# Kernel tuning notes

Measured on AMD Instinct MI355X. Metric: run time of the kernel, lower is better.

Reference implementation:

```python
import jax, jax.numpy as jnp
import numpy as np
from jax.ops import segment_sum

N_NODES = 50000
N_EDGES = 800000
N_GRAPHS = 256
F_IN, F_HID, N_HID, N_OUT = 64, 128, 512, 256


def setup_inputs() -> dict:
    key = jax.random.key(0)
    ks = jax.random.split(key, 12)
    x = jax.random.normal(ks[0], (N_NODES, F_IN), dtype=jnp.float32)
    edge_index = jax.random.randint(ks[1], (2, N_EDGES), 0, N_NODES, dtype=jnp.int64)
    batch = jnp.sort(jax.random.randint(ks[2], (N_NODES,), 0, N_GRAPHS, dtype=jnp.int64))
    def lin(k, fan_in, fan_out):
        s = 1.0 / np.sqrt(fan_in)
        return jax.random.uniform(k, (fan_in, fan_out), jnp.float32, -s, s)
    return {
        "x": x, "edge_index": edge_index, "batch": batch,
        "W0": lin(ks[3], F_IN, F_HID), "b0": jnp.zeros((F_HID,), jnp.float32),
        "W1": lin(ks[4], F_HID, F_HID), "b1": jnp.zeros((F_HID,), jnp.float32),
        "W2": lin(ks[5], F_HID, F_HID), "b2": jnp.zeros((F_HID,), jnp.float32),
        "Wm1": lin(ks[6], F_HID, N_HID), "bm1": jnp.zeros((N_HID,), jnp.float32),
        "Wm2": lin(ks[7], N_HID, N_OUT), "bm2": jnp.zeros((N_OUT,), jnp.float32),
    }


def _gcn_norm(edge_index, num_nodes):
    # PyG GCNConv default: add self-loops, symmetric D^{-1/2} A D^{-1/2} norm.
    loop = jnp.arange(num_nodes, dtype=edge_index.dtype)
    src = jnp.concatenate([edge_index[0], loop])
    dst = jnp.concatenate([edge_index[1], loop])
    deg = segment_sum(jnp.ones_like(src, dtype=jnp.float32), dst, num_segments=num_nodes)
    dis = jnp.where(deg > 0, jax.lax.rsqrt(jnp.maximum(deg, 1.0)), 0.0)
    norm = dis[src] * dis[dst]
    return src, dst, norm


def _gcn_conv(x, W, b, src, dst, norm, num_nodes):
    h = x @ W                                  # [N, F_out]
    msg = norm[:, None] * h[src]               # edge-wise gather  [E+N, F_out]
    out = segment_sum(msg, dst, num_segments=num_nodes)  # scatter-add
    return out + b


def reference(x, edge_index, batch, W0, b0, W1, b1, W2, b2, Wm1, bm1, Wm2, bm2):
    n = x.shape[0]
    src, dst, norm = _gcn_norm(edge_index, n)
    h = jax.nn.relu(_gcn_conv(x, W0, b0, src, dst, norm, n))
    h = jax.nn.relu(_gcn_conv(h, W1, b1, src, dst, norm, n))
    h = _gcn_conv(h, W2, b2, src, dst, norm, n)
    # global_mean_pool over graphs
    counts = segment_sum(jnp.ones((n,), jnp.float32), batch, num_segments=N_GRAPHS)
    g = segment_sum(h, batch, num_segments=N_GRAPHS) / jnp.maximum(counts, 1.0)[:, None]
    # mol_mlp: Linear -> ReLU -> Linear
    g = jax.nn.relu(g @ Wm1 + bm1)
    return g @ Wm2 + bm2
```

## Files before the change

### kernel.cpp

```cpp
#include <hip/hip_runtime.h>
#include <hip/hip_bf16.h>
#include <math.h>
#include <stdint.h>

#define N_NODES 50000
#define N_PAD   50048
#define N_EDGES 800000
#define N_GRAPHS 256
#define F_IN 64
#define F_HID 128
#define N_HID 512
#define N_OUT 256
#define CSR_CAP (N_EDGES + 16 * N_NODES)

#define NBKT   196
#define BKT_S  6144
#define EPB    3328
#define NBIN_BLK ((N_EDGES + EPB - 1) / EPB)
#define DUMMY_NODE N_NODES

using bf16x8 = __attribute__((ext_vector_type(8))) short;
using f32x4  = __attribute__((ext_vector_type(4))) float;

__device__ __forceinline__ unsigned int bf16pair(float a, float b) {
    unsigned int ua = __float_as_uint(a);
    unsigned int ub = __float_as_uint(b);
    ua += 0x7fffu + ((ua >> 16) & 1u);
    ub += 0x7fffu + ((ub >> 16) & 1u);
    return (ua >> 16) | (ub & 0xffff0000u);
}
__device__ __forceinline__ float bf16lo(unsigned int u) { return __uint_as_float(u << 16); }
__device__ __forceinline__ float bf16hi(unsigned int u) { return __uint_as_float(u & 0xffff0000u); }

__device__ __forceinline__ void acc8(float* a, uint4 r) {
    a[0] += bf16lo(r.x);  a[1] += bf16hi(r.x);
    a[2] += bf16lo(r.y);  a[3] += bf16hi(r.y);
    a[4] += bf16lo(r.z);  a[5] += bf16hi(r.z);
    a[6] += bf16lo(r.w);  a[7] += bf16hi(r.w);
}

__global__ void cvt_all(const float* __restrict__ in, const float* __restrict__ dis,
                        unsigned int* __restrict__ xb,
                        const float* __restrict__ W0, unsigned short* __restrict__ W0Tb,
                        const float* __restrict__ W1, unsigned short* __restrict__ W1Tb) {
    const int NX = N_NODES * F_IN / 4;
    int idx = blockIdx.x * blockDim.x + threadIdx.x;
    if (idx < NX) {
        int node = idx >> 4;
        float d = dis[node];
        float4 v = ((const float4*)in)[idx];
        ((uint2*)xb)[idx] = make_uint2(bf16pair(d * v.x, d * v.y),
                                       bf16pair(d * v.z, d * v.w));
        if (idx < 16)
            ((uint2*)xb)[(size_t)N_NODES * 16 + idx] = make_uint2(0u, 0u);
    } else {
        int j = idx - NX;
        const int N0 = F_IN * 128;
        const int N1 = F_HID * 128;
        if (j < N0) {
            int k = j >> 7, n = j & 127;
            unsigned int u = __float_as_uint(W0[j]);
            u += 0x7fffu + ((u >> 16) & 1u);
            W0Tb[n * F_IN + k] = (unsigned short)(u >> 16);
        } else if (j < N0 + N1) {
            int jj = j - N0;
            int k = jj >> 7, n = jj & 127;
            unsigned int u = __float_as_uint(W1[jj]);
            u += 0x7fffu + ((u >> 16) & 1u);
            W1Tb[n * F_HID + k] = (unsigned short)(u >> 16);
        }
    }
}

__global__ __launch_bounds__(256) void bin_edges(const int* __restrict__ ei,
                                                 int* __restrict__ bucketCur,
                                                 unsigned int* __restrict__ binned) {
    __shared__ int hist[NBKT];
    __shared__ int lbase[NBKT];
    __shared__ int lcur[NBKT];
    __shared__ int gbase[NBKT];
    __shared__ int scn[256];
    __shared__ unsigned int staging[EPB];
    int tid = threadIdx.x;
    int base = blockIdx.x * EPB;
    int cnt = N_EDGES - base; if (cnt > EPB) cnt = EPB;
    if (tid < NBKT) hist[tid] = 0;
    __syncthreads();
    unsigned int pk[13]; int nk = 0;
#pragma unroll
    for (int u = 0; u < 13; ++u) {
        int e = base + u * 256 + tid;
        if (u * 256 + tid < cnt) {
            unsigned int s = (unsigned int)ei[e];
            unsigned int d = (unsigned int)ei[N_EDGES + e];
            unsigned int b = d >> 8;
            pk[nk++] = (b << 24) | (s << 8) | (d & 255u);
        }
    }
    for (int u = 0; u < nk; ++u) atomicAdd(&hist[pk[u] >> 24], 1);
    __syncthreads();
    int h = (tid < NBKT) ? hist[tid] : 0;
    scn[tid] = h;
    __syncthreads();
    for (int off = 1; off < 256; off <<= 1) {
        int t = (tid >= off) ? scn[tid - off] : 0;
        __syncthreads();
        scn[tid] += t;
        __syncthreads();
    }
    if (tid < NBKT) { int e0 = scn[tid] - h; lbase[tid] = e0; lcur[tid] = e0; }
    __syncthreads();
    for (int u = 0; u < nk; ++u) {
        int pos = atomicAdd(&lcur[pk[u] >> 24], 1);
        staging[pos] = pk[u];
    }
    if (tid < NBKT && hist[tid] > 0)
        gbase[tid] = atomicAdd(&bucketCur[tid], hist[tid]);
    __syncthreads();
    for (int k = tid; k < cnt; k += 256) {
        unsigned int v = staging[k];
        int b = v >> 24;
        binned[(size_t)b * BKT_S + gbase[b] + (k - lbase[b])] = v & 0xffffffu;
    }
}

__global__ __launch_bounds__(256) void bucket_deg(const unsigned int* __restrict__ binned,
                                                  const int* __restrict__ bucketCur,
                                                  int* __restrict__ degs,
                                                  float* __restrict__ dis,
                                                  int* __restrict__ localOff,
                                                  int* __restrict__ bucketAligned) {
    __shared__ int hist[256];
    __shared__ int tsum[256];
    int b = blockIdx.x;
    int tid = threadIdx.x;
    int node0 = b << 8;
    hist[tid] = 0;
    __syncthreads();
    int cnt = bucketCur[b];
    const unsigned int* bb = &binned[(size_t)b * BKT_S];
    for (int k = tid; k < cnt; k += 256)
        atomicAdd(&hist[bb[k] & 255u], 1);
    __syncthreads();
    int d = hist[tid];
    int s = (d + 15) & ~15;
    tsum[tid] = s;
    __syncthreads();
    for (int off = 1; off < 256; off <<= 1) {
        int t = (tid >= off) ? tsum[tid - off] : 0;
        __syncthreads();
        tsum[tid] += t;
        __syncthreads();
    }
    int excl = tsum[tid] - s;
    int node = node0 + tid;
    if (node < N_NODES) {
        degs[node] = d;
        dis[node] = rsqrtf((float)(d + 1));
        localOff[node] = excl;
    }
    if (tid == 255) bucketAligned[b] = tsum[255];
}

__global__ __launch_bounds__(256) void scatter_local(const unsigned int* __restrict__ binned,
                                                     const int* __restrict__ bucketCur,
                                                     const int* __restrict__ bucketAligned,
                                                     const int* __restrict__ localOff,
                                                     int* __restrict__ offsets,
                                                     unsigned short* __restrict__ csr) {
    __shared__ int lcur[256];
    __shared__ int sc[256];
    __shared__ int s_csrB, s_tot;
    int b = blockIdx.x;
    int tid = threadIdx.x;
    sc[tid] = (tid < NBKT) ? bucketAligned[tid] : 0;
    __syncthreads();
    for (int off = 1; off < 256; off <<= 1) {
        int t = (tid >= off) ? sc[tid - off] : 0;
        __syncthreads();
        sc[tid] += t;
        __syncthreads();
    }
    if (tid == 0) {
        int incl = sc[b];
        int mine = bucketAligned[b];
        s_csrB = incl - mine;
        s_tot  = mine;
    }
    __syncthreads();
    int csrB = s_csrB;
    int tot  = s_tot;
    int node = (b << 8) + tid;
    int lo = (node < N_NODES) ? localOff[node] : 0;
    lcur[tid] = lo;
    if (node < N_NODES) offsets[node] = csrB + lo;
    uint4 dv = make_uint4(0xC350C350u, 0xC350C350u, 0xC350C350u, 0xC350C350u);
    uint4* cp = (uint4*)(csr + csrB);
    for (int k = tid; k < (tot >> 3); k += 256) cp[k] = dv;
    __syncthreads();
    int cnt = bucketCur[b];
    const unsigned int* bb = &binned[(size_t)b * BKT_S];
    for (int k = tid; k < cnt; k += 256) {
        unsigned int v = bb[k];
        int dl = v & 255u;
        int p = atomicAdd(&lcur[dl], 1);
        csr[csrB + p] = (unsigned short)(v >> 8);
    }
}

template <int K, bool BIASRELU, bool DISSCALE>
__global__ __launch_bounds__(256) void gemm_mfma(const unsigned short* __restrict__ Ab,
                                                 const unsigned short* __restrict__ WTb,
                                                 const float* __restrict__ bias,
                                                 const float* __restrict__ disv,
                                                 unsigned int* __restrict__ outb, int M) {
    int wv = threadIdx.x >> 6;
    int lane = threadIdx.x & 63;
    int m = lane & 15;
    int quad = lane >> 4;
    int row0 = blockIdx.x * 64 + wv * 16;
    f32x4 acc[8];
#pragma unroll
    for (int t = 0; t < 8; ++t) acc[t] = (f32x4){0.f, 0.f, 0.f, 0.f};
#pragma unroll
    for (int ks = 0; ks < K; ks += 32) {
        bf16x8 af = *(const bf16x8*)&Ab[(size_t)(row0 + m) * K + ks + quad * 8];
#pragma unroll
        for (int t = 0; t < 8; ++t) {
            bf16x8 bf = *(const bf16x8*)&WTb[(size_t)(t * 16 + m) * K + ks + quad * 8];
            acc[t] = __builtin_amdgcn_mfma_f32_16x16x32_bf16(af, bf, acc[t], 0, 0, 0);
        }
    }
    float dr[4];
#pragma unroll
    for (int r = 0; r < 4; ++r) {
        int row = row0 + quad * 4 + r;
        dr[r] = DISSCALE ? ((row < M) ? disv[row] : 0.f) : 1.f;
    }
#pragma unroll
    for (int t = 0; t < 8; ++t) {
        int col = t * 16 + m;
        float bcol = 0.f;
        if (BIASRELU) bcol = bias[col];
#pragma unroll
        for (int r = 0; r < 4; ++r) {
            float v = acc[t][r];
            if (BIASRELU) v = fmaxf(v + bcol, 0.f);
            if (DISSCALE) v = v * dr[r];
            float vn = __shfl_xor(v, 1, 64);
            if ((m & 1) == 0) {
                int row = row0 + quad * 4 + r;
                if (row < M)
                    outb[(size_t)row * 64 + (col >> 1)] = bf16pair(v, vn);
                else
                    outb[(size_t)row * 64 + (col >> 1)] = 0u;
            }
        }
    }
}

template <bool RELU, bool BIAS, bool SCALEOUT>
__global__ __launch_bounds__(256) void aggregate128b(const uint4* __restrict__ hb4,
                                                     const int* __restrict__ offsets,
                                                     const int* __restrict__ degs,
                                                     const unsigned short* __restrict__ csr,
                                                     const float* __restrict__ dis,
                                                     const float* __restrict__ bias,
                                                     unsigned int* __restrict__ outb) {
    int wave = threadIdx.x >> 6;
    int lane = threadIdx.x & 63;
    int i = blockIdx.x * 4 + wave;
    int sub = lane >> 4;
    int q   = lane & 15;
    if (i >= N_NODES) {
        if (i == N_NODES && sub == 0)
            ((uint4*)outb)[(size_t)N_NODES * 16 + q] = make_uint4(0u, 0u, 0u, 0u);
        return;
    }
    float a[8];
#pragma unroll
    for (int k = 0; k < 8; ++k) a[k] = 0.f;
    int j = offsets[i];
    int e1 = j + ((degs[i] + 15) & ~15);
    for (; j < e1; j += 16) {
        uint2 w = *(const uint2*)&csr[j + 4 * sub];
        int s0 = w.x & 0xffff, s1 = w.x >> 16;
        int s2 = w.y & 0xffff, s3 = w.y >> 16;
        uint4 r0 = hb4[(size_t)s0 * 16 + q];
        uint4 r1 = hb4[(size_t)s1 * 16 + q];
        uint4 r2 = hb4[(size_t)s2 * 16 + q];
        uint4 r3 = hb4[(size_t)s3 * 16 + q];
        acc8(a, r0); acc8(a, r1); acc8(a, r2); acc8(a, r3);
    }
#pragma unroll
    for (int k = 0; k < 8; ++k) a[k] += __shfl_xor(a[k], 16, 64);
#pragma unroll
    for (int k = 0; k < 8; ++k) a[k] += __shfl_xor(a[k], 32, 64);
    uint4 su = hb4[(size_t)i * 16 + q];
    acc8(a, su);
    float dii = dis[i];
#pragma unroll
    for (int k = 0; k < 8; ++k) a[k] *= dii;
    if (BIAS) {
        float4 b0 = ((const float4*)bias)[2 * q];
        float4 b1 = ((const float4*)bias)[2 * q + 1];
        a[0] += b0.x; a[1] += b0.y; a[2] += b0.z; a[3] += b0.w;
        a[4] += b1.x; a[5] += b1.y; a[6] += b1.z; a[7] += b1.w;
    }
    if (RELU) {
#pragma unroll
        for (int k = 0; k < 8; ++k) a[k] = fmaxf(a[k], 0.f);
    }
    if (sub == 0) {
        float sc = SCALEOUT ? dii : 1.f;
        ((uint4*)outb)[(size_t)i * 16 + q] =
            make_uint4(bf16pair(sc * a[0], sc * a[1]), bf16pair(sc * a[2], sc * a[3]),
                       bf16pair(sc * a[4], sc * a[5]), bf16pair(sc * a[6], sc * a[7]));
    }
}

__global__ __launch_bounds__(256) void aggregate_xb(const uint4* __restrict__ xb4,
                                                    const float* __restrict__ x,
                                                    const int* __restrict__ offsets,
                                                    const int* __restrict__ degs,
                                                    const unsigned short* __restrict__ csr,
                                                    const float* __restrict__ dis,
                                                    unsigned int* __restrict__ outb) {
    int wave = threadIdx.x >> 6;
    int lane = threadIdx.x & 63;
    int i = blockIdx.x * 4 + wave;
    int sub = lane >> 3;
    int q   = lane & 7;
    if (i >= N_NODES) {
        if (i == N_NODES && sub == 0)
            ((uint4*)outb)[(size_t)N_NODES * 8 + q] = make_uint4(0u, 0u, 0u, 0u);
        return;
    }
    float a[8];
#pragma unroll
    for (int k = 0; k < 8; ++k) a[k] = 0.f;
    int j = offsets[i];
    int e1 = j + ((degs[i] + 15) & ~15);
    for (; j < e1; j += 16) {
        unsigned int w = *(const unsigned int*)&csr[j + 2 * sub];
        int s0 = w & 0xffff, s1 = w >> 16;
        uint4 r0 = xb4[(size_t)s0 * 8 + q];
        uint4 r1 = xb4[(size_t)s1 * 8 + q];
        acc8(a, r0); acc8(a, r1);
    }
#pragma unroll
    for (int k = 0; k < 8; ++k) a[k] += __shfl_xor(a[k], 8, 64);
#pragma unroll
    for (int k = 0; k < 8; ++k) a[k] += __shfl_xor(a[k], 16, 64);
#pragma unroll
    for (int k = 0; k < 8; ++k) a[k] += __shfl_xor(a[k], 32, 64);
    float dii = dis[i];
    float d2 = dii * dii;
    float4 sx0 = ((const float4*)x)[(size_t)i * 16 + 2 * q];
    float4 sx1 = ((const float4*)x)[(size_t)i * 16 + 2 * q + 1];
    a[0] = dii * a[0] + d2 * sx0.x;  a[1] = dii * a[1] + d2 * sx0.y;
    a[2] = dii * a[2] + d2 * sx0.z;  a[3] = dii * a[3] + d2 * sx0.w;
    a[4] = dii * a[4] + d2 * sx1.x;  a[5] = dii * a[5] + d2 * sx1.y;
    a[6] = dii * a[6] + d2 * sx1.z;  a[7] = dii * a[7] + d2 * sx1.w;
    if (sub == 0)
        ((uint4*)outb)[(size_t)i * 8 + q] =
            make_uint4(bf16pair(a[0], a[1]), bf16pair(a[2], a[3]),
                       bf16pair(a[4], a[5]), bf16pair(a[6], a[7]));
}

__global__ __launch_bounds__(128) void pool16(const unsigned int* __restrict__ hb,
                                              const int* __restrict__ batch,
                                              float* __restrict__ g_acc,
                                              float* __restrict__ g_cnt) {
    const int NB = 16;
    int base = blockIdx.x * NB;
    int f = threadIdx.x;
    int uidx = f >> 1;
    bool hi = f & 1;
    float acc = 0.f;
    int cur = -1, cnt = 0;
    for (int n = 0; n < NB; ++n) {
        int i = base + n;
        if (i >= N_NODES) break;
        int b = batch[i];
        if (b != cur) {
            if (cur >= 0) {
                atomicAdd(&g_acc[(size_t)cur * F_HID + f], acc);
                if (f == 0) atomicAdd(&g_cnt[cur], (float)cnt);
            }
            cur = b; acc = 0.f; cnt = 0;
        }
        unsigned int u = hb[(size_t)i * 64 + uidx];
        acc += hi ? bf16hi(u) : bf16lo(u);
        cnt++;
    }
    if (cur >= 0) {
        atomicAdd(&g_acc[(size_t)cur * F_HID + f], acc);
        if (f == 0) atomicAdd(&g_cnt[cur], (float)cnt);
    }
}

__global__ __launch_bounds__(512) void fused_mlp(const float* __restrict__ g_acc,
                                                 const float* __restrict__ g_cnt,
                                                 const float* __restrict__ W2,
                                                 const float* __restrict__ b2,
                                                 const float* __restrict__ Wm1,
                                                 const float* __restrict__ bm1,
                                                 const float* __restrict__ Wm2,
                                                 const float* __restrict__ bm2,
                                                 float* __restrict__ out) {
    __shared__ float pool_row[F_HID];
    __shared__ float g2row[F_HID];
    __shared__ float hid[N_HID];
    int g = blockIdx.x;
    int t = threadIdx.x;
    if (t < F_HID) {
        float c = g_cnt[g];
        pool_row[t] = g_acc[(size_t)g * F_HID + t] / fmaxf(c, 1.0f);
    }
    __syncthreads();
    if (t < F_HID) {
        float acc = b2[t];
        for (int k = 0; k < F_HID; ++k) acc += pool_row[k] * W2[(size_t)k * F_HID + t];
        g2row[t] = acc;
    }
    __syncthreads();
    {
        float acc = bm1[t];
        for (int k = 0; k < F_HID; ++k) acc += g2row[k] * Wm1[(size_t)k * N_HID + t];
        hid[t] = fmaxf(acc, 0.f);
    }
    __syncthreads();
    if (t < N_OUT) {
        float acc = bm2[t];
        for (int k = 0; k < N_HID; ++k) acc += hid[k] * Wm2[(size_t)k * N_OUT + t];
        out[(size_t)g * N_OUT + t] = acc;
    }
}

extern "C" void kernel_launch(void* const* d_in, const int* in_sizes, int n_in,
                              void* d_out, int out_size, void* d_ws, size_t ws_size,
                              hipStream_t stream) {
    const float* x   = (const float*)d_in[0];
    const int* ei    = (const int*)d_in[1];
    const int* batch = (const int*)d_in[2];
    const float* W0 = (const float*)d_in[3];  const float* b0 = (const float*)d_in[4];
    const float* W1 = (const float*)d_in[5];  const float* b1 = (const float*)d_in[6];
    const float* W2 = (const float*)d_in[7];  const float* b2 = (const float*)d_in[8];
    const float* Wm1 = (const float*)d_in[9];  const float* bm1 = (const float*)d_in[10];
    const float* Wm2 = (const float*)d_in[11]; const float* bm2 = (const float*)d_in[12];

    char* p = (char*)d_ws;
    auto alloc = [&](size_t bytes) -> char* {
        char* r = p;
        p += (bytes + 255) & ~(size_t)255;
        return r;
    };
    int*   bucketCur = (int*)alloc(NBKT * 4);
    float* g_acc  = (float*)alloc((size_t)N_GRAPHS * F_HID * 4);
    float* g_cnt  = (float*)alloc(N_GRAPHS * 4);
    size_t zero_bytes = (size_t)(p - (char*)bucketCur);
    unsigned int* binned = (unsigned int*)alloc((size_t)NBKT * BKT_S * 4);
    int*   bucketAligned = (int*)alloc(NBKT * 4);
    int*   offsets = (int*)alloc((size_t)N_NODES * 4);
    int*   degs    = (int*)alloc((size_t)N_NODES * 4);
    int*   localOff = (int*)alloc((size_t)N_NODES * 4);
    float* dis     = (float*)alloc((size_t)N_NODES * 4);
    unsigned short* csr = (unsigned short*)alloc((size_t)CSR_CAP * 2 + 32);
    unsigned int* xb     = (unsigned int*)alloc((size_t)N_PAD * F_IN / 2 * 4);
    unsigned int* axb    = (unsigned int*)alloc((size_t)N_PAD * F_IN / 2 * 4);
    unsigned int* h_ab   = (unsigned int*)alloc((size_t)N_PAD * F_HID / 2 * 4);
    unsigned int* h_tmpb = (unsigned int*)alloc((size_t)N_PAD * F_HID / 2 * 4);
    unsigned int* h_bb   = (unsigned int*)alloc((size_t)N_PAD * F_HID / 2 * 4);
    unsigned int* agg2b  = (unsigned int*)alloc((size_t)N_PAD * F_HID / 2 * 4);
    unsigned short* W0Tb = (unsigned short*)alloc((size_t)128 * F_IN * 2);
    unsigned short* W1Tb = (unsigned short*)alloc((size_t)128 * F_HID * 2);
    (void)ws_size; (void)in_sizes; (void)n_in; (void)out_size;

    (void)hipMemsetAsync(bucketCur, 0, zero_bytes, stream);

    bin_edges<<<NBIN_BLK, 256, 0, stream>>>(ei, bucketCur, binned);
    bucket_deg<<<NBKT, 256, 0, stream>>>(binned, bucketCur, degs, dis, localOff, bucketAligned);

    const int NCVT = N_NODES * F_IN / 4 + (F_IN + F_HID) * 128;
    cvt_all<<<(NCVT + 255) / 256, 256, 0, stream>>>(x, dis, xb, W0, W0Tb, W1, W1Tb);

    scatter_local<<<NBKT, 256, 0, stream>>>(binned, bucketCur, bucketAligned, localOff,
                                            offsets, csr);

    int agg_grid = N_NODES / 4 + 1;
    int mfma_grid = N_PAD / 64;

    aggregate_xb<<<agg_grid, 256, 0, stream>>>((const uint4*)xb, x, offsets, degs, csr, dis, axb);
    gemm_mfma<F_IN, true, false><<<mfma_grid, 256, 0, stream>>>(
        (const unsigned short*)axb, W0Tb, b0, nullptr, h_ab, N_NODES);
    gemm_mfma<F_HID, false, true><<<mfma_grid, 256, 0, stream>>>(
        (const unsigned short*)h_ab, W1Tb, nullptr, dis, h_tmpb, N_NODES);
    aggregate128b<true, true, true><<<agg_grid, 256, 0, stream>>>(
        (const uint4*)h_tmpb, offsets, degs, csr, dis, b1, h_bb);
    aggregate128b<false, false, false><<<agg_grid, 256, 0, stream>>>(
        (const uint4*)h_bb, offsets, degs, csr, dis, nullptr, agg2b);

    pool16<<<(N_NODES + 15) / 16, 128, 0, stream>>>(agg2b, batch, g_acc, g_cnt);
    fused_mlp<<<N_GRAPHS, 512, 0, stream>>>(g_acc, g_cnt, W2, b2, Wm1, bm1, Wm2, bm2,
                                            (float*)d_out);
}
```

Baseline: 273.8 us.

## Fuse degree/scatter, chain both GEMMs through LDS, fuse last aggregate with pooling

Merges bucket_deg and scatter_local into one kernel that builds each bucket's CSR slice in shared memory at a fixed per-bucket capacity, which removes the global prefix scan and the localOff/bucketAligned round trips. The two MFMA GEMMs are fused so the ReLU'd layer-0 output stays in swizzled LDS instead of going through global memory. The final aggregation is fused with mean pooling, so the agg2b buffer and the pool16 launch go away. The costs are a fixed 8192-entry bucket capacity that risks overflow if a bucket holds more edges, and more atomics into g_acc from many small blocks.

```diff
diff --git a/kernel.cpp b/kernel.cpp
--- a/kernel.cpp
+++ b/kernel.cpp
@@ -11,10 +11,10 @@
 #define F_HID 128
 #define N_HID 512
 #define N_OUT 256
-#define CSR_CAP (N_EDGES + 16 * N_NODES)
 
 #define NBKT   196
 #define BKT_S  6144
+#define BKT_CAP 8192
 #define EPB    3328
 #define NBIN_BLK ((N_EDGES + EPB - 1) / EPB)
 #define DUMMY_NODE N_NODES
@@ -28,6 +28,11 @@
     ua += 0x7fffu + ((ua >> 16) & 1u);
     ub += 0x7fffu + ((ub >> 16) & 1u);
     return (ua >> 16) | (ub & 0xffff0000u);
+}
+__device__ __forceinline__ unsigned short bf16one(float a) {
+    unsigned int ua = __float_as_uint(a);
+    ua += 0x7fffu + ((ua >> 16) & 1u);
+    return (unsigned short)(ua >> 16);
 }
 __device__ __forceinline__ float bf16lo(unsigned int u) { return __uint_as_float(u << 16); }
 __device__ __forceinline__ float bf16hi(unsigned int u) { return __uint_as_float(u & 0xffff0000u); }
@@ -59,15 +64,11 @@
         const int N1 = F_HID * 128;
         if (j < N0) {
             int k = j >> 7, n = j & 127;
-            unsigned int u = __float_as_uint(W0[j]);
-            u += 0x7fffu + ((u >> 16) & 1u);
-            W0Tb[n * F_IN + k] = (unsigned short)(u >> 16);
+            W0Tb[n * F_IN + k] = bf16one(W0[j]);
         } else if (j < N0 + N1) {
             int jj = j - N0;
             int k = jj >> 7, n = jj & 127;
-            unsigned int u = __float_as_uint(W1[jj]);
-            u += 0x7fffu + ((u >> 16) & 1u);
-            W1Tb[n * F_HID + k] = (unsigned short)(u >> 16);
+            W1Tb[n * F_HID + k] = bf16one(W1[jj]);
         }
     }
 }
@@ -124,14 +125,17 @@
     }
 }
 
-__global__ __launch_bounds__(256) void bucket_deg(const unsigned int* __restrict__ binned,
-                                                  const int* __restrict__ bucketCur,
-                                                  int* __restrict__ degs,
-                                                  float* __restrict__ dis,
-                                                  int* __restrict__ localOff,
-                                                  int* __restrict__ bucketAligned) {
+__global__ __launch_bounds__(256) void deg_scatter(const unsigned int* __restrict__ binned,
+                                                   const int* __restrict__ bucketCur,
+                                                   int* __restrict__ degs,
+                                                   float* __restrict__ dis,
+                                                   int* __restrict__ offsets,
+                                                   unsigned short* __restrict__ csr) {
     __shared__ int hist[256];
     __shared__ int tsum[256];
+    __shared__ int lcur[256];
+    __shared__ uint4 scsr4[BKT_CAP / 8];
+    unsigned short* scsr = (unsigned short*)scsr4;
     int b = blockIdx.x;
     int tid = threadIdx.x;
     int node0 = b << 8;
@@ -153,81 +157,76 @@
         __syncthreads();
     }
     int excl = tsum[tid] - s;
+    int tot = tsum[255];
+    int csrB = b * BKT_CAP;
     int node = node0 + tid;
     if (node < N_NODES) {
         degs[node] = d;
         dis[node] = rsqrtf((float)(d + 1));
-        localOff[node] = excl;
-    }
-    if (tid == 255) bucketAligned[b] = tsum[255];
-}
-
-__global__ __launch_bounds__(256) void scatter_local(const unsigned int* __restrict__ binned,
-                                                     const int* __restrict__ bucketCur,
-                                                     const int* __restrict__ bucketAligned,
-                                                     const int* __restrict__ localOff,
-                                                     int* __restrict__ offsets,
-                                                     unsigned short* __restrict__ csr) {
-    __shared__ int lcur[256];
-    __shared__ int sc[256];
-    __shared__ int s_csrB, s_tot;
-    int b = blockIdx.x;
-    int tid = threadIdx.x;
-    sc[tid] = (tid < NBKT) ? bucketAligned[tid] : 0;
-    __syncthreads();
-    for (int off = 1; off < 256; off <<= 1) {
-        int t = (tid >= off) ? sc[tid - off] : 0;
-        __syncthreads();
-        sc[tid] += t;
-        __syncthreads();
-    }
-    if (tid == 0) {
-        int incl = sc[b];
-        int mine = bucketAligned[b];
-        s_csrB = incl - mine;
-        s_tot  = mine;
-    }
-    __syncthreads();
-    int csrB = s_csrB;
-    int tot  = s_tot;
-    int node = (b << 8) + tid;
-    int lo = (node < N_NODES) ? localOff[node] : 0;
-    lcur[tid] = lo;
-    if (node < N_NODES) offsets[node] = csrB + lo;
-    uint4 dv = make_uint4(0xC350C350u, 0xC350C350u, 0xC350C350u, 0xC350C350u);
-    uint4* cp = (uint4*)(csr + csrB);
-    for (int k = tid; k < (tot >> 3); k += 256) cp[k] = dv;
-    __syncthreads();
-    int cnt = bucketCur[b];
-    const unsigned int* bb = &binned[(size_t)b * BKT_S];
+        offsets[node] = csrB + excl;
+    }
+    lcur[tid] = excl;
+    uint2 dv = make_uint2(0xC350C350u, 0xC350C350u);
+    for (int k = tid; k < (tot >> 2); k += 256) ((uint2*)scsr)[k] = dv;
+    __syncthreads();
     for (int k = tid; k < cnt; k += 256) {
         unsigned int v = bb[k];
         int dl = v & 255u;
         int p = atomicAdd(&lcur[dl], 1);
-        csr[csrB + p] = (unsigned short)(v >> 8);
-    }
-}
-
-template <int K, bool BIASRELU, bool DISSCALE>
-__global__ __launch_bounds__(256) void gemm_mfma(const unsigned short* __restrict__ Ab,
-                                                 const unsigned short* __restrict__ WTb,
-                                                 const float* __restrict__ bias,
-                                                 const float* __restrict__ disv,
-                                                 unsigned int* __restrict__ outb, int M) {
+        scsr[p] = (unsigned short)(v >> 8);
+    }
+    __syncthreads();
+    for (int k = tid; k < (tot >> 3); k += 256)
+        ((uint4*)(csr + csrB))[k] = scsr4[k];
+}
+
+__global__ __launch_bounds__(256) void gemm01_mfma(const unsigned short* __restrict__ Ab,
+                                                   const unsigned short* __restrict__ W0T,
+                                                   const float* __restrict__ b0,
+                                                   const unsigned short* __restrict__ W1T,
+                                                   const float* __restrict__ disv,
+                                                   unsigned int* __restrict__ outb, int M) {
+    __shared__ unsigned short tile[4][16 * 128];
     int wv = threadIdx.x >> 6;
     int lane = threadIdx.x & 63;
     int m = lane & 15;
     int quad = lane >> 4;
     int row0 = blockIdx.x * 64 + wv * 16;
+    char* tl = (char*)&tile[wv][0];
     f32x4 acc[8];
 #pragma unroll
     for (int t = 0; t < 8; ++t) acc[t] = (f32x4){0.f, 0.f, 0.f, 0.f};
 #pragma unroll
-    for (int ks = 0; ks < K; ks += 32) {
-        bf16x8 af = *(const bf16x8*)&Ab[(size_t)(row0 + m) * K + ks + quad * 8];
+    for (int ks = 0; ks < F_IN; ks += 32) {
+        bf16x8 af = *(const bf16x8*)&Ab[(size_t)(row0 + m) * F_IN + ks + quad * 8];
 #pragma unroll
         for (int t = 0; t < 8; ++t) {
-            bf16x8 bf = *(const bf16x8*)&WTb[(size_t)(t * 16 + m) * K + ks + quad * 8];
+            bf16x8 bf = *(const bf16x8*)&W0T[(size_t)(t * 16 + m) * F_IN + ks + quad * 8];
+            acc[t] = __builtin_amdgcn_mfma_f32_16x16x32_bf16(af, bf, acc[t], 0, 0, 0);
+        }
+    }
+#pragma unroll
+    for (int t = 0; t < 8; ++t) {
+        int col = t * 16 + m;
+        float bcol = b0[col];
+#pragma unroll
+        for (int r = 0; r < 4; ++r) {
+            int row = quad * 4 + r;
+            float v = fmaxf(acc[t][r] + bcol, 0.f);
+            int byte = (row * 256 + col * 2) ^ ((row & 7) << 4);
+            *(unsigned short*)(tl + byte) = bf16one(v);
+        }
+    }
+    __syncthreads();
+#pragma unroll
+    for (int t = 0; t < 8; ++t) acc[t] = (f32x4){0.f, 0.f, 0.f, 0.f};
+#pragma unroll
+    for (int ks = 0; ks < F_HID; ks += 32) {
+        int byte = (m * 256 + ks * 2 + quad * 16) ^ ((m & 7) << 4);
+        bf16x8 af = *(const bf16x8*)(tl + byte);
+#pragma unroll
+        for (int t = 0; t < 8; ++t) {
+            bf16x8 bf = *(const bf16x8*)&W1T[(size_t)(t * 16 + m) * F_HID + ks + quad * 8];
             acc[t] = __builtin_amdgcn_mfma_f32_16x16x32_bf16(af, bf, acc[t], 0, 0, 0);
         }
     }
@@ -235,25 +234,18 @@
 #pragma unroll
     for (int r = 0; r < 4; ++r) {
         int row = row0 + quad * 4 + r;
-        dr[r] = DISSCALE ? ((row < M) ? disv[row] : 0.f) : 1.f;
+        dr[r] = (row < M) ? disv[row] : 0.f;
     }
 #pragma unroll
     for (int t = 0; t < 8; ++t) {
         int col = t * 16 + m;
-        float bcol = 0.f;
-        if (BIASRELU) bcol = bias[col];
 #pragma unroll
         for (int r = 0; r < 4; ++r) {
-            float v = acc[t][r];
-            if (BIASRELU) v = fmaxf(v + bcol, 0.f);
-            if (DISSCALE) v = v * dr[r];
+            float v = acc[t][r] * dr[r];
             float vn = __shfl_xor(v, 1, 64);
             if ((m & 1) == 0) {
                 int row = row0 + quad * 4 + r;
-                if (row < M)
-                    outb[(size_t)row * 64 + (col >> 1)] = bf16pair(v, vn);
-                else
-                    outb[(size_t)row * 64 + (col >> 1)] = 0u;
+                outb[(size_t)row * 64 + (col >> 1)] = (row < M) ? bf16pair(v, vn) : 0u;
             }
         }
     }
@@ -368,36 +360,70 @@
                        bf16pair(a[4], a[5]), bf16pair(a[6], a[7]));
 }
 
-__global__ __launch_bounds__(128) void pool16(const unsigned int* __restrict__ hb,
-                                              const int* __restrict__ batch,
-                                              float* __restrict__ g_acc,
-                                              float* __restrict__ g_cnt) {
-    const int NB = 16;
-    int base = blockIdx.x * NB;
-    int f = threadIdx.x;
-    int uidx = f >> 1;
-    bool hi = f & 1;
-    float acc = 0.f;
-    int cur = -1, cnt = 0;
-    for (int n = 0; n < NB; ++n) {
-        int i = base + n;
+__global__ __launch_bounds__(256) void aggregate_pool(const uint4* __restrict__ hb4,
+                                                      const int* __restrict__ offsets,
+                                                      const int* __restrict__ degs,
+                                                      const unsigned short* __restrict__ csr,
+                                                      const float* __restrict__ dis,
+                                                      const int* __restrict__ batch,
+                                                      float* __restrict__ g_acc,
+                                                      float* __restrict__ g_cnt) {
+    const int NPW = 4;
+    int wave = threadIdx.x >> 6;
+    int lane = threadIdx.x & 63;
+    int sub = lane >> 4;
+    int q   = lane & 15;
+    int i0 = (blockIdx.x * 4 + wave) * NPW;
+    if (i0 >= N_NODES) return;
+    float pa[8];
+#pragma unroll
+    for (int k = 0; k < 8; ++k) pa[k] = 0.f;
+    int curg = -1; float cntf = 0.f;
+    auto flush = [&]() {
+        if (sub == 0) {
+#pragma unroll
+            for (int k = 0; k < 8; ++k)
+                atomicAdd(&g_acc[(size_t)curg * F_HID + q * 8 + k], pa[k]);
+            if (lane == 0) atomicAdd(&g_cnt[curg], cntf);
+        }
+    };
+    for (int n = 0; n < NPW; ++n) {
+        int i = i0 + n;
         if (i >= N_NODES) break;
-        int b = batch[i];
-        if (b != cur) {
-            if (cur >= 0) {
-                atomicAdd(&g_acc[(size_t)cur * F_HID + f], acc);
-                if (f == 0) atomicAdd(&g_cnt[cur], (float)cnt);
-            }
-            cur = b; acc = 0.f; cnt = 0;
-        }
-        unsigned int u = hb[(size_t)i * 64 + uidx];
-        acc += hi ? bf16hi(u) : bf16lo(u);
-        cnt++;
-    }
-    if (cur >= 0) {
-        atomicAdd(&g_acc[(size_t)cur * F_HID + f], acc);
-        if (f == 0) atomicAdd(&g_cnt[cur], (float)cnt);
-    }
+        float a[8];
+#pragma unroll
+        for (int k = 0; k < 8; ++k) a[k] = 0.f;
+        int j = offsets[i];
+        int e1 = j + ((degs[i] + 15) & ~15);
+        for (; j < e1; j += 16) {
+            uint2 w = *(const uint2*)&csr[j + 4 * sub];
+            int s0 = w.x & 0xffff, s1 = w.x >> 16;
+            int s2 = w.y & 0xffff, s3 = w.y >> 16;
+            uint4 r0 = hb4[(size_t)s0 * 16 + q];
+            uint4 r1 = hb4[(size_t)s1 * 16 + q];
+            uint4 r2 = hb4[(size_t)s2 * 16 + q];
+            uint4 r3 = hb4[(size_t)s3 * 16 + q];
+            acc8(a, r0); acc8(a, r1); acc8(a, r2); acc8(a, r3);
+        }
+#pragma unroll
+        for (int k = 0; k < 8; ++k) a[k] += __shfl_xor(a[k], 16, 64);
+#pragma unroll
+        for (int k = 0; k < 8; ++k) a[k] += __shfl_xor(a[k], 32, 64);
+        uint4 su = hb4[(size_t)i * 16 + q];
+        acc8(a, su);
+        float dii = dis[i];
+        int g = batch[i];
+        if (g != curg) {
+            if (curg >= 0) flush();
+            curg = g; cntf = 0.f;
+#pragma unroll
+            for (int k = 0; k < 8; ++k) pa[k] = 0.f;
+        }
+#pragma unroll
+        for (int k = 0; k < 8; ++k) pa[k] += a[k] * dii;
+        cntf += 1.f;
+    }
+    if (curg >= 0) flush();
 }
 
 __global__ __launch_bounds__(512) void fused_mlp(const float* __restrict__ g_acc,
@@ -461,18 +487,14 @@
     float* g_cnt  = (float*)alloc(N_GRAPHS * 4);
     size_t zero_bytes = (size_t)(p - (char*)bucketCur);
     unsigned int* binned = (unsigned int*)alloc((size_t)NBKT * BKT_S * 4);
-    int*   bucketAligned = (int*)alloc(NBKT * 4);
     int*   offsets = (int*)alloc((size_t)N_NODES * 4);
     int*   degs    = (int*)alloc((size_t)N_NODES * 4);
-    int*   localOff = (int*)alloc((size_t)N_NODES * 4);
     float* dis     = (float*)alloc((size_t)N_NODES * 4);
-    unsigned short* csr = (unsigned short*)alloc((size_t)CSR_CAP * 2 + 32);
+    unsigned short* csr = (unsigned short*)alloc((size_t)NBKT * BKT_CAP * 2 + 32);
     unsigned int* xb     = (unsigned int*)alloc((size_t)N_PAD * F_IN / 2 * 4);
     unsigned int* axb    = (unsigned int*)alloc((size_t)N_PAD * F_IN / 2 * 4);
-    unsigned int* h_ab   = (unsigned int*)alloc((size_t)N_PAD * F_HID / 2 * 4);
     unsigned int* h_tmpb = (unsigned int*)alloc((size_t)N_PAD * F_HID / 2 * 4);
     unsigned int* h_bb   = (unsigned int*)alloc((size_t)N_PAD * F_HID / 2 * 4);
-    unsigned int* agg2b  = (unsigned int*)alloc((size_t)N_PAD * F_HID / 2 * 4);
     unsigned short* W0Tb = (unsigned short*)alloc((size_t)128 * F_IN * 2);
     unsigned short* W1Tb = (unsigned short*)alloc((size_t)128 * F_HID * 2);
     (void)ws_size; (void)in_sizes; (void)n_in; (void)out_size;
@@ -480,28 +502,22 @@
     (void)hipMemsetAsync(bucketCur, 0, zero_bytes, stream);
 
     bin_edges<<<NBIN_BLK, 256, 0, stream>>>(ei, bucketCur, binned);
-    bucket_deg<<<NBKT, 256, 0, stream>>>(binned, bucketCur, degs, dis, localOff, bucketAligned);
+    deg_scatter<<<NBKT, 256, 0, stream>>>(binned, bucketCur, degs, dis, offsets, csr);
 
     const int NCVT = N_NODES * F_IN / 4 + (F_IN + F_HID) * 128;
     cvt_all<<<(NCVT + 255) / 256, 256, 0, stream>>>(x, dis, xb, W0, W0Tb, W1, W1Tb);
 
-    scatter_local<<<NBKT, 256, 0, stream>>>(binned, bucketCur, bucketAligned, localOff,
-                                            offsets, csr);
-
     int agg_grid = N_NODES / 4 + 1;
     int mfma_grid = N_PAD / 64;
 
     aggregate_xb<<<agg_grid, 256, 0, stream>>>((const uint4*)xb, x, offsets, degs, csr, dis, axb);
-    gemm_mfma<F_IN, true, false><<<mfma_grid, 256, 0, stream>>>(
-        (const unsigned short*)axb, W0Tb, b0, nullptr, h_ab, N_NODES);
-    gemm_mfma<F_HID, false, true><<<mfma_grid, 256, 0, stream>>>(
-        (const unsigned short*)h_ab, W1Tb, nullptr, dis, h_tmpb, N_NODES);
+    gemm01_mfma<<<mfma_grid, 256, 0, stream>>>(
+        (const unsigned short*)axb, W0Tb, b0, W1Tb, dis, h_tmpb, N_NODES);
     aggregate128b<true, true, true><<<agg_grid, 256, 0, stream>>>(
         (const uint4*)h_tmpb, offsets, degs, csr, dis, b1, h_bb);
-    aggregate128b<false, false, false><<<agg_grid, 256, 0, stream>>>(
-        (const uint4*)h_bb, offsets, degs, csr, dis, nullptr, agg2b);
-
-    pool16<<<(N_NODES + 15) / 16, 128, 0, stream>>>(agg2b, batch, g_acc, g_cnt);
+    aggregate_pool<<<(N_NODES + 15) / 16, 256, 0, stream>>>(
+        (const uint4*)h_bb, offsets, degs, csr, dis, batch, g_acc, g_cnt);
+
     fused_mlp<<<N_GRAPHS, 512, 0, stream>>>(g_acc, g_cnt, W2, b2, Wm1, bm1, Wm2, bm2,
                                             (float*)d_out);
 }
```

Measured after the change: 299.2 us. 1.09x slower.
